# Kernel optimization log

Hardware: AMD Instinct MI355X
Metric: run time of the kernel (lower is better)

The kernel has to match this reference:

```python
import jax, jax.numpy as jnp
import numpy as np

NEG_BIG = -9e15


def gat_layer(h, adj, W, a, alpha, concat):
    # h: (N, Fin), W: (Fin, Fout), a: (2*Fout, 1)
    Wh = h @ W                                   # (N, Fout)
    F = Wh.shape[1]
    # e[i,j] = LeakyReLU(cat(Wh_i, Wh_j) @ a) = LeakyReLU(s_i + d_j)
    s = Wh @ a[:F, 0]                            # (N,)
    d = Wh @ a[F:, 0]                            # (N,)
    e = jax.nn.leaky_relu(s[:, None] + d[None, :], negative_slope=alpha)  # (N, N)
    e = jnp.where(adj > 0, e, NEG_BIG)
    att = jax.nn.softmax(e, axis=1)              # (N, N)
    out = att @ Wh                               # (N, Fout)
    return jax.nn.elu(out) if concat else out


def setup_inputs() -> dict:
    key = jax.random.key(0)
    ks = jax.random.split(key, 12)
    N, nfeat, nhid, nlatent, nclass = 8192, 512, 256, 64, 16

    def xavier(k, shape):
        gain = 1.414
        fan_in, fan_out = shape[0], shape[1]
        bound = gain * np.sqrt(6.0 / (fan_in + fan_out))
        return jax.random.uniform(k, shape, jnp.float32, -bound, bound)

    x = jax.random.normal(ks[0], (N, nfeat), jnp.float32)
    adj = jax.random.randint(ks[1], (N, N), 0, 2, jnp.int32)
    eps = jax.random.normal(ks[2], (N, nlatent), jnp.float32)
    return {
        "x": x,
        "adj": adj,
        "eps": eps,
        "W1": xavier(ks[3], (nfeat, nhid)),
        "a1": xavier(ks[4], (2 * nhid, 1)),
        "Wmu": xavier(ks[5], (nhid, nlatent)),
        "amu": xavier(ks[6], (2 * nlatent, 1)),
        "Wlv": xavier(ks[7], (nhid, nlatent)),
        "alv": xavier(ks[8], (2 * nlatent, 1)),
        "Wc": xavier(ks[9], (nlatent, nclass)),
        "bc": jnp.zeros((nclass,), jnp.float32),
    }


def reference(x, adj, eps, W1, a1, Wmu, amu, Wlv, alv, Wc, bc):
    alpha = 0.2  # LeakyReLU negative slope
    # eval mode: all dropouts are identity
    h = gat_layer(x, adj, W1, a1, alpha, concat=True)      # (N, nhid)
    mu = gat_layer(h, adj, Wmu, amu, alpha, concat=False)  # (N, nlatent)
    logvar = gat_layer(h, adj, Wlv, alv, alpha, concat=False)
    z = mu + eps * jnp.exp(0.5 * logvar)
    logits = z @ Wc + bc                                   # (N, nclass)
    return logits, mu, logvar
```

## Files before the change

### kernel.cpp

```cpp
#include <hip/hip_runtime.h>

typedef unsigned short u16;
typedef __attribute__((ext_vector_type(8))) short short8;
typedef __attribute__((ext_vector_type(4))) float f32x4;

#define NROW 8192

__device__ __forceinline__ float bf2f(u16 h) {
  unsigned u = ((unsigned)h) << 16;
  return __builtin_bit_cast(float, u);
}
__device__ __forceinline__ float ldf(const void* p, size_t i, int f32) {
  return f32 ? ((const float*)p)[i] : bf2f(((const u16*)p)[i]);
}
__device__ __forceinline__ u16 f2bf(float f) {
  unsigned b = __builtin_bit_cast(unsigned, f);
  b += 0x7FFFu + ((b >> 16) & 1u);
  return (u16)(b >> 16);
}

__global__ void detect3(const u16* __restrict__ xr, unsigned* __restrict__ mode) {
  __shared__ int zc, bg;
  int t = threadIdx.x;
  if (t == 0) { zc = 0; bg = 0; }
  __syncthreads();
  int zeros_even = 0; int big = 0;
  for (int i = t; i < 4096; i += 256) {
    u16 v = xr[i];
    if (!(i & 1) && v == 0) zeros_even++;
    if (fabsf(bf2f(v)) > 1e6f) big = 1;
  }
  atomicAdd(&zc, zeros_even);
  if (big) atomicOr(&bg, 1);
  __syncthreads();
  if (t == 0) *mode = (zc > 512 || bg) ? 1u : 0u;
}

__global__ void detect_adj(const unsigned* __restrict__ a, unsigned* __restrict__ amode) {
  __shared__ int clo;
  int t = threadIdx.x;
  if (t == 0) clo = 0;
  __syncthreads();
  int c = 0;
  for (int i = t; i < 4096; i += 256)
    if (a[i] == 0x00003F80u) c++;
  atomicAdd(&clo, c);
  __syncthreads();
  if (t == 0) *amode = (clo > 32) ? 1u : 0u;
}

__global__ __launch_bounds__(256) void adj_bits(const void* __restrict__ adj,
    unsigned char* __restrict__ bits, const unsigned* __restrict__ amodep) {
  int amode = (int)*amodep;
  for (size_t b = (size_t)blockIdx.x * 256 + threadIdx.x; b < 8388608; b += 524288) {
    size_t e0 = b * 8;
    unsigned byte = 0;
    if (amode == 0) {
      int4 a0 = *(const int4*)((const int*)adj + e0);
      int4 a1 = *(const int4*)((const int*)adj + e0 + 4);
      byte = (a0.x != 0) | ((a0.y != 0) << 1) | ((a0.z != 0) << 2) | ((a0.w != 0) << 3) |
             ((a1.x != 0) << 4) | ((a1.y != 0) << 5) | ((a1.z != 0) << 6) | ((a1.w != 0) << 7);
    } else {
      ushort4 a0 = *(const ushort4*)((const u16*)adj + e0);
      ushort4 a1 = *(const ushort4*)((const u16*)adj + e0 + 4);
      byte = (a0.x != 0) | ((a0.y != 0) << 1) | ((a0.z != 0) << 2) | ((a0.w != 0) << 3) |
             ((a1.x != 0) << 4) | ((a1.y != 0) << 5) | ((a1.z != 0) << 6) | ((a1.w != 0) << 7);
    }
    bits[b] = (unsigned char)byte;
  }
}

__global__ __launch_bounds__(256) void gemm_mfma(const u16* __restrict__ Abf,
    const u16* __restrict__ BT, float* __restrict__ C, int K, int N) {
  int tid = threadIdx.x;
  int l = tid & 63, w = tid >> 6;
  int m0 = blockIdx.y * 64, n0 = blockIdx.x * 64;
  const u16* arow = Abf + (size_t)(m0 + w * 16 + (l & 15)) * K + (l >> 4) * 8;
  const u16* brow = BT + (size_t)(n0 + (l & 15)) * K + (l >> 4) * 8;
  f32x4 acc[4];
#pragma unroll
  for (int nt = 0; nt < 4; ++nt) acc[nt] = (f32x4){0.f, 0.f, 0.f, 0.f};
  for (int k0 = 0; k0 < K; k0 += 32) {
    short8 a = *(const short8*)(arow + k0);
#pragma unroll
    for (int nt = 0; nt < 4; ++nt) {
      short8 b = *(const short8*)(brow + (size_t)nt * 16 * K + k0);
      acc[nt] = __builtin_amdgcn_mfma_f32_16x16x32_bf16(a, b, acc[nt], 0, 0, 0);
    }
  }
#pragma unroll
  for (int nt = 0; nt < 4; ++nt)
#pragma unroll
    for (int q = 0; q < 4; ++q)
      C[(size_t)(m0 + w * 16 + (l >> 4) * 4 + q) * N + n0 + nt * 16 + (l & 15)] =
          acc[nt][q];
}

__global__ __launch_bounds__(256) void gemm2_dual(const u16* __restrict__ Abf,
    const u16* __restrict__ BT0, const u16* __restrict__ BT1,
    float* __restrict__ C0, float* __restrict__ C1) {
  const int K = 256, N = 64;
  const u16* BT = blockIdx.x ? BT1 : BT0;
  float* C = blockIdx.x ? C1 : C0;
  int tid = threadIdx.x, l = tid & 63, w = tid >> 6;
  int m0 = blockIdx.y * 64;
  const u16* arow = Abf + (size_t)(m0 + w * 16 + (l & 15)) * K + (l >> 4) * 8;
  const u16* brow = BT + (size_t)(l & 15) * K + (l >> 4) * 8;
  f32x4 acc[4];
#pragma unroll
  for (int nt = 0; nt < 4; ++nt) acc[nt] = (f32x4){0.f, 0.f, 0.f, 0.f};
  for (int k0 = 0; k0 < K; k0 += 32) {
    short8 a = *(const short8*)(arow + k0);
#pragma unroll
    for (int nt = 0; nt < 4; ++nt) {
      short8 b = *(const short8*)(brow + (size_t)nt * 16 * K + k0);
      acc[nt] = __builtin_amdgcn_mfma_f32_16x16x32_bf16(a, b, acc[nt], 0, 0, 0);
    }
  }
#pragma unroll
  for (int nt = 0; nt < 4; ++nt)
#pragma unroll
    for (int q = 0; q < 4; ++q)
      C[(size_t)(m0 + w * 16 + (l >> 4) * 4 + q) * N + nt * 16 + (l & 15)] = acc[nt][q];
}

__global__ __launch_bounds__(256) void convert_bf16(const void* __restrict__ in,
    u16* __restrict__ out, int n8, const unsigned* __restrict__ modep) {
  int f32 = (int)*modep;
  int i = blockIdx.x * 256 + threadIdx.x;
  if (i >= n8) return;
  if (f32) {
    float4 v0 = ((const float4*)in)[(size_t)i * 2];
    float4 v1 = ((const float4*)in)[(size_t)i * 2 + 1];
    ushort4 o0 = {f2bf(v0.x), f2bf(v0.y), f2bf(v0.z), f2bf(v0.w)};
    ushort4 o1 = {f2bf(v1.x), f2bf(v1.y), f2bf(v1.z), f2bf(v1.w)};
    ((ushort4*)out)[(size_t)i * 2] = o0;
    ((ushort4*)out)[(size_t)i * 2 + 1] = o1;
  } else {
    ((int4*)out)[i] = ((const int4*)in)[i];
  }
}

__global__ __launch_bounds__(256) void transpose_bf16(const float* __restrict__ in,
    u16* __restrict__ out, int M, int F) {
  __shared__ float t[32][33];
  int m0 = blockIdx.x * 32, f0 = blockIdx.y * 32;
  int c = threadIdx.x & 31, r = threadIdx.x >> 5;
  for (int rr = r; rr < 32; rr += 8)
    t[rr][c] = in[(size_t)(m0 + rr) * F + f0 + c];
  __syncthreads();
  for (int rr = r; rr < 32; rr += 8)
    out[(size_t)(f0 + rr) * M + m0 + c] = f2bf(t[c][rr]);
}

__global__ __launch_bounds__(256) void transpose_any(const void* __restrict__ in,
    u16* __restrict__ out, int M, int F, const unsigned* __restrict__ modep) {
  int f32 = (int)*modep;
  __shared__ u16 t[32][33];
  int m0 = blockIdx.x * 32, f0 = blockIdx.y * 32;
  int c = threadIdx.x & 31, r = threadIdx.x >> 5;
  for (int rr = r; rr < 32; rr += 8)
    t[rr][c] = f2bf(ldf(in, (size_t)(m0 + rr) * F + f0 + c, f32));
  __syncthreads();
  for (int rr = r; rr < 32; rr += 8)
    out[(size_t)(f0 + rr) * M + m0 + c] = t[c][rr];
}

__global__ __launch_bounds__(256) void transpose_w2(const void* __restrict__ in0,
    const void* __restrict__ in1, u16* __restrict__ out0, u16* __restrict__ out1,
    int M, int F, const unsigned* __restrict__ modep) {
  int f32 = (int)*modep;
  const void* in = blockIdx.z ? in1 : in0;
  u16* out = blockIdx.z ? out1 : out0;
  __shared__ u16 t[32][33];
  int m0 = blockIdx.x * 32, f0 = blockIdx.y * 32;
  int c = threadIdx.x & 31, r = threadIdx.x >> 5;
  for (int rr = r; rr < 32; rr += 8)
    t[rr][c] = f2bf(ldf(in, (size_t)(m0 + rr) * F + f0 + c, f32));
  __syncthreads();
  for (int rr = r; rr < 32; rr += 8)
    out[(size_t)(f0 + rr) * M + m0 + c] = t[c][rr];
}

__global__ __launch_bounds__(256) void transpose_pair(const float* __restrict__ in0,
    const float* __restrict__ in1, u16* __restrict__ out0, u16* __restrict__ out1,
    int M, int F) {
  const float* in = blockIdx.z ? in1 : in0;
  u16* out = blockIdx.z ? out1 : out0;
  __shared__ float t[32][33];
  int m0 = blockIdx.x * 32, f0 = blockIdx.y * 32;
  int c = threadIdx.x & 31, r = threadIdx.x >> 5;
  for (int rr = r; rr < 32; rr += 8)
    t[rr][c] = in[(size_t)(m0 + rr) * F + f0 + c];
  __syncthreads();
  for (int rr = r; rr < 32; rr += 8)
    out[(size_t)(f0 + rr) * M + m0 + c] = f2bf(t[c][rr]);
}

__global__ __launch_bounds__(256) void sd_f32(const float* __restrict__ Wh,
    const void* __restrict__ a2, float* __restrict__ s, float* __restrict__ d,
    int F, const unsigned* __restrict__ modep) {
  int f32 = (int)*modep;
  int row = blockIdx.x * 4 + (threadIdx.x >> 6);
  int l = threadIdx.x & 63;
  float ss = 0.f, dd = 0.f;
  for (int k = l; k < F; k += 64) {
    float wv = Wh[(size_t)row * F + k];
    ss += wv * ldf(a2, k, f32);
    dd += wv * ldf(a2, F + k, f32);
  }
#pragma unroll
  for (int off = 32; off > 0; off >>= 1) {
    ss += __shfl_down(ss, off, 64);
    dd += __shfl_down(dd, off, 64);
  }
  if (l == 0) { s[row] = ss; d[row] = dd; }
}

__global__ __launch_bounds__(256) void sd_dual(const float* __restrict__ Wh0,
    const float* __restrict__ Wh1, const void* __restrict__ a0,
    const void* __restrict__ a1, float* __restrict__ s0, float* __restrict__ s1,
    float* __restrict__ d0, float* __restrict__ d1,
    const unsigned* __restrict__ modep) {
  int f32 = (int)*modep;
  int L = blockIdx.y;
  const float* Wh = L ? Wh1 : Wh0;
  const void* a2 = L ? a1 : a0;
  int row = blockIdx.x * 4 + (threadIdx.x >> 6);
  int l = threadIdx.x & 63;
  float wv = Wh[(size_t)row * 64 + l];
  float ss = wv * ldf(a2, l, f32);
  float dd = wv * ldf(a2, 64 + l, f32);
#pragma unroll
  for (int off = 32; off > 0; off >>= 1) {
    ss += __shfl_down(ss, off, 64);
    dd += __shfl_down(dd, off, 64);
  }
  if (l == 0) { (L ? s1 : s0)[row] = ss; (L ? d1 : d0)[row] = dd; }
}

__global__ __launch_bounds__(256) void dmax_reduce(const float* __restrict__ da,
    const float* __restrict__ db, float* __restrict__ cells) {
  const float* d = blockIdx.x ? db : da;
  __shared__ float red[256];
  float m = -3.4e38f;
  for (int i = threadIdx.x; i < NROW; i += 256) m = fmaxf(m, d[i]);
  red[threadIdx.x] = m;
  __syncthreads();
#pragma unroll
  for (int sft = 128; sft > 0; sft >>= 1) {
    if (threadIdx.x < sft) red[threadIdx.x] = fmaxf(red[threadIdx.x], red[threadIdx.x + sft]);
    __syncthreads();
  }
  if (threadIdx.x == 0) cells[blockIdx.x * 16] = red[0];
}

template <int NL>
__global__ __launch_bounds__(512, 2) void flash_v2(
    const u16* __restrict__ whTa, const u16* __restrict__ whTb,
    const float* __restrict__ sa, const float* __restrict__ da,
    const float* __restrict__ sb, const float* __restrict__ db,
    const float* __restrict__ cella, const float* __restrict__ cellb,
    const unsigned char* __restrict__ abits,
    void* __restrict__ o0, void* __restrict__ o1,
    void* __restrict__ o2, void* __restrict__ o3) {
  constexpr int FDIM = (NL == 1) ? 256 : 64;
  constexpr int NT = FDIM / 16;
  constexpr int NW_L = (NL == 1) ? 8 : 4;
  constexpr int JSL = NROW / NW_L;
  constexpr int NKS = JSL / 32;
  __shared__ __align__(16) float dd_[NL][NROW];
  __shared__ float lsp[8][32];
  __shared__ float ls_[NL][32];
  int tid = threadIdx.x, l = tid & 63, w = tid >> 6;
  int r0 = blockIdx.x * 32;
  int layer = (NL == 1) ? 0 : (w >> 2);
  int wl = (NL == 1) ? w : (w & 3);
  for (int u = tid; u < NL * (NROW / 4); u += 512) {
    int L = u / (NROW / 4), uu = u - L * (NROW / 4);
    ((float4*)dd_[L])[uu] = ((const float4*)(L ? db : da))[uu];
  }
  __syncthreads();
  const u16* whT = layer ? whTb : whTa;
  const float* sW = layer ? sb : sa;
  const float* ddp = dd_[layer];
  float Dm = layer ? *cellb : *cella;
  int rlo = r0 + (l & 15);
  float sv0 = sW[rlo], sv1 = sW[rlo + 16];
  float t0 = sv0 + Dm, t1 = sv1 + Dm;
  float Ms0 = fmaxf(t0, 0.2f * t0), Ms1 = fmaxf(t1, 0.2f * t1);
  int jsbase = wl * JSL;
  int koff = (l >> 4) * 8;
  const uint4* pb0 = (const uint4*)(abits + (size_t)rlo * 1024 + (jsbase >> 3));
  const uint4* pb1 = (const uint4*)(abits + (size_t)(rlo + 16) * 1024 + (jsbase >> 3));
  f32x4 acc[2][NT];
#pragma unroll
  for (int m = 0; m < 2; ++m)
#pragma unroll
    for (int n = 0; n < NT; ++n) acc[m][n] = (f32x4){0.f, 0.f, 0.f, 0.f};
  float psum0 = 0.f, psum1 = 0.f;
  int bsh = (l >> 4) * 8;
  uint4 aw0 = pb0[0], aw1 = pb1[0];
  for (int g = 0; g < NKS / 4; ++g) {
    uint4 c0 = aw0, c1 = aw1;
    if (g + 1 < NKS / 4) { aw0 = pb0[g + 1]; aw1 = pb1[g + 1]; }
    unsigned wd0[4] = {c0.x, c0.y, c0.z, c0.w};
    unsigned wd1[4] = {c1.x, c1.y, c1.z, c1.w};
#pragma unroll
    for (int kk = 0; kk < 4; ++kk) {
      int j0 = jsbase + (g * 4 + kk) * 32;
      unsigned ab0 = (wd0[kk] >> bsh) & 0xffu;
      unsigned ab1 = (wd1[kk] >> bsh) & 0xffu;
      float4 dv0 = *(const float4*)&ddp[j0 + koff];
      float4 dv1 = *(const float4*)&ddp[j0 + koff + 4];
      float dvv[8] = {dv0.x, dv0.y, dv0.z, dv0.w, dv1.x, dv1.y, dv1.z, dv1.w};
      short8 af0, af1;
#pragma unroll
      for (int q = 0; q < 8; ++q) {
        float a0 = sv0 + dvv[q];
        float e0 = fmaxf(a0, 0.2f * a0) - Ms0;
        float p0 = ((ab0 >> q) & 1u) ? __expf(e0) : 0.f;
        psum0 += p0;
        af0[q] = (short)f2bf(p0);
        float a1 = sv1 + dvv[q];
        float e1 = fmaxf(a1, 0.2f * a1) - Ms1;
        float p1 = ((ab1 >> q) & 1u) ? __expf(e1) : 0.f;
        psum1 += p1;
        af1[q] = (short)f2bf(p1);
      }
      size_t jc = (size_t)(j0 + koff);
#pragma unroll
      for (int nt = 0; nt < NT; ++nt) {
        short8 b = *(const short8*)&whT[(size_t)(nt * 16 + (l & 15)) * NROW + jc];
        acc[0][nt] = __builtin_amdgcn_mfma_f32_16x16x32_bf16(af0, b, acc[0][nt], 0, 0, 0);
        acc[1][nt] = __builtin_amdgcn_mfma_f32_16x16x32_bf16(af1, b, acc[1][nt], 0, 0, 0);
      }
    }
  }
  psum0 += __shfl_xor(psum0, 16, 64); psum0 += __shfl_xor(psum0, 32, 64);
  psum1 += __shfl_xor(psum1, 16, 64); psum1 += __shfl_xor(psum1, 32, 64);
  if (l < 16) { lsp[w][l] = psum0; lsp[w][16 + l] = psum1; }
  __syncthreads();
  if (tid < 32 * NL) {
    int L = tid >> 5, r = tid & 31;
    float t = 0.f;
#pragma unroll
    for (int wv = 0; wv < NW_L; ++wv) t += lsp[L * NW_L + wv][r];
    ls_[L][r] = t;
  }
  __syncthreads();
  float* red = (float*)dd_;
  if constexpr (NL == 1) {
    u16* hb = (u16*)o0;
#pragma unroll
    for (int cg = 0; cg < 8; ++cg) {
#pragma unroll
      for (int mh = 0; mh < 2; ++mh)
#pragma unroll
        for (int ntl = 0; ntl < 2; ++ntl)
#pragma unroll
          for (int q = 0; q < 4; ++q)
            red[w * 1024 + (mh * 16 + (l >> 4) * 4 + q) * 32 + ntl * 16 + (l & 15)] =
                acc[mh][cg * 2 + ntl][q];
      __syncthreads();
      for (int e = tid; e < 1024; e += 512) {
        int r = e >> 5, c = e & 31;
        float x = 0.f;
#pragma unroll
        for (int wv = 0; wv < 8; ++wv) x += red[wv * 1024 + r * 32 + c];
        x /= ls_[0][r];
        x = (x > 0.f) ? x : (__expf(x) - 1.f);
        hb[(size_t)(r0 + r) * 256 + cg * 32 + c] = f2bf(x);
      }
      __syncthreads();
    }
  } else {
#pragma unroll
    for (int mh = 0; mh < 2; ++mh)
#pragma unroll
      for (int nt = 0; nt < 4; ++nt)
#pragma unroll
        for (int q = 0; q < 4; ++q)
          red[layer * 8192 + wl * 2048 + (mh * 16 + (l >> 4) * 4 + q) * 64 +
              nt * 16 + (l & 15)] = acc[mh][nt][q];
    __syncthreads();
    for (int e = tid; e < 4096; e += 512) {
      int L = e >> 11, rc = e & 2047, r = rc >> 6, c = rc & 63;
      float x = 0.f;
#pragma unroll
      for (int wv = 0; wv < 4; ++wv) x += red[L * 8192 + wv * 2048 + r * 64 + c];
      x /= ls_[L][r];
      size_t gi = (size_t)(r0 + r) * 64 + c;
      ((float*)(L ? o2 : o0))[gi] = x;
      ((float*)(L ? o3 : o1))[gi] = x;
    }
  }
}

__global__ __launch_bounds__(256) void logits_f32(const float* __restrict__ mu,
    const float* __restrict__ lv, const void* __restrict__ eps,
    const void* __restrict__ Wc, const void* __restrict__ bcv,
    float* __restrict__ outL, const unsigned* __restrict__ modep) {
  int f32 = (int)*modep;
  __shared__ float zs[32 * 64];
  __shared__ float wcs[64 * 16];
  int tid = threadIdx.x;
  for (int i = tid; i < 1024; i += 256) wcs[i] = ldf(Wc, i, f32);
  int row0 = blockIdx.x * 32;
  for (int i = tid; i < 2048; i += 256) {
    int r = i >> 6, c = i & 63;
    size_t g = (size_t)(row0 + r) * 64 + c;
    zs[i] = mu[g] + ldf(eps, g, f32) * __expf(0.5f * lv[g]);
  }
  __syncthreads();
  for (int it = tid; it < 512; it += 256) {
    int r = it >> 4, oc = it & 15;
    float a = ldf(bcv, oc, f32);
    for (int c = 0; c < 64; ++c) a += zs[r * 64 + c] * wcs[c * 16 + oc];
    outL[(size_t)(row0 + r) * 16 + oc] = a;
  }
}

extern "C" void kernel_launch(void* const* d_in, const int* in_sizes, int n_in,
                              void* d_out, int out_size, void* d_ws, size_t ws_size,
                              hipStream_t stream) {
  (void)out_size; (void)ws_size;
  int ix = 0, iadj = 1, ieps = 2, iW1 = 3, ia1 = 4, iWmu = 5, iamu = 6,
      iWlv = 7, ialv = 8, iWc = 9, ibc = 10;
  {
    int fmu = -1, flv = -1, fam = -1, fal = -1;
    for (int i = 0; i < n_in; ++i) {
      switch (in_sizes[i]) {
        case 67108864: iadj = i; break;
        case 4194304:  ix   = i; break;
        case 524288:   ieps = i; break;
        case 131072:   iW1  = i; break;
        case 512:      ia1  = i; break;
        case 1024:     iWc  = i; break;
        case 16:       ibc  = i; break;
        case 16384:    if (fmu < 0) fmu = i; else flv = i; break;
        case 128:      if (fam < 0) fam = i; else fal = i; break;
        default: break;
      }
    }
    if (fmu >= 0 && flv >= 0) { iWmu = fmu; iWlv = flv; }
    if (fam >= 0 && fal >= 0) { iamu = fam; ialv = fal; }
  }
  const void* adj = d_in[iadj];
  char* ws = (char*)d_ws;
  const size_t KB = 1024, MB = 1024 * 1024;
  float* wh1   = (float*)(ws + 0);
  float* whmu  = (float*)(ws + 0);
  float* whlv  = (float*)(ws + 2 * MB);
  float* muf   = (float*)(ws + 4 * MB);
  float* lvf   = (float*)(ws + 6 * MB);
  u16*   xbf   = (u16*)(ws + 8 * MB);
  u16*   whT1  = (u16*)(ws + 8 * MB);
  u16*   hbf   = (u16*)(ws + 12 * MB);
  u16*   whmuT = (u16*)(ws + 20 * MB);
  u16*   whlvT = (u16*)(ws + 21 * MB);
  u16*   W1T   = (u16*)(ws + 22 * MB);
  u16*   WmuT  = (u16*)(ws + 22 * MB + 256 * KB);
  u16*   WlvT  = (u16*)(ws + 22 * MB + 288 * KB);
  float* s1    = (float*)(ws + 24 * MB + 96 * KB);
  float* d1    = (float*)(ws + 24 * MB + 128 * KB);
  float* smu   = (float*)(ws + 24 * MB + 160 * KB);
  float* dmu   = (float*)(ws + 24 * MB + 192 * KB);
  float* slv   = (float*)(ws + 24 * MB + 224 * KB);
  float* dlv   = (float*)(ws + 24 * MB + 256 * KB);
  float* dmaxv = (float*)(ws + 24 * MB + 288 * KB);
  unsigned* mode  = (unsigned*)(ws + 24 * MB + 289 * KB);
  unsigned* amode = (unsigned*)(ws + 24 * MB + 290 * KB);
  unsigned char* abits = (unsigned char*)(ws + 25 * MB);

  float* out_logits = (float*)d_out;
  float* out_mu     = (float*)d_out + 131072;
  float* out_lv     = (float*)d_out + 655360;

  detect3<<<1, 256, 0, stream>>>((const u16*)d_in[ix], mode);
  detect_adj<<<1, 256, 0, stream>>>((const unsigned*)adj, amode);
  adj_bits<<<2048, 256, 0, stream>>>(adj, abits, amode);

  convert_bf16<<<2048, 256, 0, stream>>>(d_in[ix], xbf, 524288, mode);
  transpose_any<<<dim3(16, 8), 256, 0, stream>>>(d_in[iW1], W1T, 512, 256, mode);
  gemm_mfma<<<dim3(4, 128), 256, 0, stream>>>(xbf, W1T, wh1, 512, 256);
  transpose_bf16<<<dim3(256, 8), 256, 0, stream>>>(wh1, whT1, 8192, 256);
  sd_f32<<<2048, 256, 0, stream>>>(wh1, d_in[ia1], s1, d1, 256, mode);
  dmax_reduce<<<1, 256, 0, stream>>>(d1, d1, dmaxv + 0);
  flash_v2<1><<<256, 512, 0, stream>>>(whT1, nullptr, s1, d1,
      nullptr, nullptr, dmaxv + 0, nullptr, abits,
      hbf, nullptr, nullptr, nullptr);

  transpose_w2<<<dim3(8, 2, 2), 256, 0, stream>>>(d_in[iWmu], d_in[iWlv],
      WmuT, WlvT, 256, 64, mode);
  gemm2_dual<<<dim3(2, 128), 256, 0, stream>>>(hbf, WmuT, WlvT, whmu, whlv);
  transpose_pair<<<dim3(256, 2, 2), 256, 0, stream>>>(whmu, whlv, whmuT, whlvT,
      8192, 64);
  sd_dual<<<dim3(2048, 2), 256, 0, stream>>>(whmu, whlv, d_in[iamu], d_in[ialv],
      smu, slv, dmu, dlv, mode);
  dmax_reduce<<<2, 256, 0, stream>>>(dmu, dlv, dmaxv + 16);
  flash_v2<2><<<256, 512, 0, stream>>>(whmuT, whlvT, smu, dmu, slv, dlv,
      dmaxv + 16, dmaxv + 32, abits,
      muf, out_mu, lvf, out_lv);

  logits_f32<<<256, 256, 0, stream>>>(muf, lvf, d_in[ieps], d_in[iWc], d_in[ibc], out_logits, mode);
}
```

Baseline: 757.2 us.

## Split layer-1 attention waves across feature halves instead of key slices

For the first GAT layer, the eight waves per block now form four key slices times two feature halves of 128 columns each. Previously they were eight key slices over all 256 features. Each wave holds half as many accumulators, and the launch bound drops to one block per SM so the compiler has more registers. The cost is that both feature halves recompute the same exponentials and masks for their key slice, and the cross-wave reduction now works per half.

```diff
diff --git a/kernel.cpp b/kernel.cpp
--- a/kernel.cpp
+++ b/kernel.cpp
@@ -256,7 +256,7 @@
 }
 
 template <int NL>
-__global__ __launch_bounds__(512, 2) void flash_v2(
+__global__ __launch_bounds__(512, 1) void flash_v3(
     const u16* __restrict__ whTa, const u16* __restrict__ whTb,
     const float* __restrict__ sa, const float* __restrict__ da,
     const float* __restrict__ sb, const float* __restrict__ db,
@@ -265,9 +265,8 @@
     void* __restrict__ o0, void* __restrict__ o1,
     void* __restrict__ o2, void* __restrict__ o3) {
   constexpr int FDIM = (NL == 1) ? 256 : 64;
-  constexpr int NT = FDIM / 16;
-  constexpr int NW_L = (NL == 1) ? 8 : 4;
-  constexpr int JSL = NROW / NW_L;
+  constexpr int NT = (NL == 1) ? 8 : 4;
+  constexpr int JSL = 2048;
   constexpr int NKS = JSL / 32;
   __shared__ __align__(16) float dd_[NL][NROW];
   __shared__ float lsp[8][32];
@@ -275,7 +274,9 @@
   int tid = threadIdx.x, l = tid & 63, w = tid >> 6;
   int r0 = blockIdx.x * 32;
   int layer = (NL == 1) ? 0 : (w >> 2);
-  int wl = (NL == 1) ? w : (w & 3);
+  int js = w & 3;
+  int nh = (NL == 1) ? (w >> 2) : 0;
+  int ntbase = nh * 8;
   for (int u = tid; u < NL * (NROW / 4); u += 512) {
     int L = u / (NROW / 4), uu = u - L * (NROW / 4);
     ((float4*)dd_[L])[uu] = ((const float4*)(L ? db : da))[uu];
@@ -289,7 +290,7 @@
   float sv0 = sW[rlo], sv1 = sW[rlo + 16];
   float t0 = sv0 + Dm, t1 = sv1 + Dm;
   float Ms0 = fmaxf(t0, 0.2f * t0), Ms1 = fmaxf(t1, 0.2f * t1);
-  int jsbase = wl * JSL;
+  int jsbase = js * JSL;
   int koff = (l >> 4) * 8;
   const uint4* pb0 = (const uint4*)(abits + (size_t)rlo * 1024 + (jsbase >> 3));
   const uint4* pb1 = (const uint4*)(abits + (size_t)(rlo + 16) * 1024 + (jsbase >> 3));
@@ -331,7 +332,7 @@
       size_t jc = (size_t)(j0 + koff);
 #pragma unroll
       for (int nt = 0; nt < NT; ++nt) {
-        short8 b = *(const short8*)&whT[(size_t)(nt * 16 + (l & 15)) * NROW + jc];
+        short8 b = *(const short8*)&whT[(size_t)((ntbase + nt) * 16 + (l & 15)) * NROW + jc];
         acc[0][nt] = __builtin_amdgcn_mfma_f32_16x16x32_bf16(af0, b, acc[0][nt], 0, 0, 0);
         acc[1][nt] = __builtin_amdgcn_mfma_f32_16x16x32_bf16(af1, b, acc[1][nt], 0, 0, 0);
       }
@@ -339,13 +340,15 @@
   }
   psum0 += __shfl_xor(psum0, 16, 64); psum0 += __shfl_xor(psum0, 32, 64);
   psum1 += __shfl_xor(psum1, 16, 64); psum1 += __shfl_xor(psum1, 32, 64);
-  if (l < 16) { lsp[w][l] = psum0; lsp[w][16 + l] = psum1; }
+  bool wlead = (NL == 1) ? (nh == 0) : true;
+  int lspi = (NL == 1) ? js : (layer * 4 + js);
+  if (l < 16 && wlead) { lsp[lspi][l] = psum0; lsp[lspi][16 + l] = psum1; }
   __syncthreads();
   if (tid < 32 * NL) {
     int L = tid >> 5, r = tid & 31;
     float t = 0.f;
 #pragma unroll
-    for (int wv = 0; wv < NW_L; ++wv) t += lsp[L * NW_L + wv][r];
+    for (int wv = 0; wv < 4; ++wv) t += lsp[L * 4 + wv][r];
     ls_[L][r] = t;
   }
   __syncthreads();
@@ -353,24 +356,24 @@
   if constexpr (NL == 1) {
     u16* hb = (u16*)o0;
 #pragma unroll
-    for (int cg = 0; cg < 8; ++cg) {
+    for (int cgl = 0; cgl < 4; ++cgl) {
 #pragma unroll
       for (int mh = 0; mh < 2; ++mh)
 #pragma unroll
         for (int ntl = 0; ntl < 2; ++ntl)
 #pragma unroll
           for (int q = 0; q < 4; ++q)
-            red[w * 1024 + (mh * 16 + (l >> 4) * 4 + q) * 32 + ntl * 16 + (l & 15)] =
-                acc[mh][cg * 2 + ntl][q];
+            red[nh * 4096 + js * 1024 + (mh * 16 + (l >> 4) * 4 + q) * 32 +
+                ntl * 16 + (l & 15)] = acc[mh][cgl * 2 + ntl][q];
       __syncthreads();
-      for (int e = tid; e < 1024; e += 512) {
-        int r = e >> 5, c = e & 31;
+      for (int e = tid; e < 2048; e += 512) {
+        int nh2 = e >> 10, rc = e & 1023, r = rc >> 5, c = rc & 31;
         float x = 0.f;
 #pragma unroll
-        for (int wv = 0; wv < 8; ++wv) x += red[wv * 1024 + r * 32 + c];
+        for (int wv = 0; wv < 4; ++wv) x += red[nh2 * 4096 + wv * 1024 + r * 32 + c];
         x /= ls_[0][r];
         x = (x > 0.f) ? x : (__expf(x) - 1.f);
-        hb[(size_t)(r0 + r) * 256 + cg * 32 + c] = f2bf(x);
+        hb[(size_t)(r0 + r) * 256 + nh2 * 128 + cgl * 32 + c] = f2bf(x);
       }
       __syncthreads();
     }
@@ -381,7 +384,7 @@
       for (int nt = 0; nt < 4; ++nt)
 #pragma unroll
         for (int q = 0; q < 4; ++q)
-          red[layer * 8192 + wl * 2048 + (mh * 16 + (l >> 4) * 4 + q) * 64 +
+          red[layer * 8192 + js * 2048 + (mh * 16 + (l >> 4) * 4 + q) * 64 +
               nt * 16 + (l & 15)] = acc[mh][nt][q];
     __syncthreads();
     for (int e = tid; e < 4096; e += 512) {
@@ -487,7 +490,7 @@
   transpose_bf16<<<dim3(256, 8), 256, 0, stream>>>(wh1, whT1, 8192, 256);
   sd_f32<<<2048, 256, 0, stream>>>(wh1, d_in[ia1], s1, d1, 256, mode);
   dmax_reduce<<<1, 256, 0, stream>>>(d1, d1, dmaxv + 0);
-  flash_v2<1><<<256, 512, 0, stream>>>(whT1, nullptr, s1, d1,
+  flash_v3<1><<<256, 512, 0, stream>>>(whT1, nullptr, s1, d1,
       nullptr, nullptr, dmaxv + 0, nullptr, abits,
       hbf, nullptr, nullptr, nullptr);
 
@@ -499,7 +502,7 @@
   sd_dual<<<dim3(2048, 2), 256, 0, stream>>>(whmu, whlv, d_in[iamu], d_in[ialv],
       smu, slv, dmu, dlv, mode);
   dmax_reduce<<<2, 256, 0, stream>>>(dmu, dlv, dmaxv + 16);
-  flash_v2<2><<<256, 512, 0, stream>>>(whmuT, whlvT, smu, dmu, slv, dlv,
+  flash_v3<2><<<256, 512, 0, stream>>>(whmuT, whlvT, smu, dmu, slv, dlv,
       dmaxv + 16, dmaxv + 32, abits,
       muf, out_mu, lvf, out_lv);
 
```

New measurement: 692.4 us. 1.09x faster.
